# Kernel tuning notes

Hardware: AMD Instinct MI355X
Metric: run time of the kernel (lower is better)

The kernel has to match this reference:

```python
import jax, jax.numpy as jnp
import numpy as np

NUM_USERS, NUM_ITEMS, D = 100000, 200000, 128
B, LLEN, SLEN = 4096, 200, 50
NEG = -1e9


def setup_inputs() -> dict:
    key = jax.random.key(0)
    ks = jax.random.split(key, 10)
    w_range = float(np.sqrt(3.0 / D))
    return {
        "user_table": 0.01 * jax.random.normal(ks[0], (NUM_USERS, D), dtype=jnp.float32),
        "item_table": 0.01 * jax.random.normal(ks[1], (NUM_ITEMS, D), dtype=jnp.float32),
        "W1": jax.random.uniform(ks[2], (2 * D, 16), minval=-w_range, maxval=w_range, dtype=jnp.float32),
        "b1": jnp.zeros((16,), dtype=jnp.float32),
        "W2": jax.random.uniform(ks[3], (16, 1), minval=-w_range, maxval=w_range, dtype=jnp.float32),
        "b2": jnp.zeros((1,), dtype=jnp.float32),
        "user_inputs": jax.random.randint(ks[4], (B,), 0, NUM_USERS, dtype=jnp.int64) if jax.config.jax_enable_x64 else jax.random.randint(ks[4], (B,), 0, NUM_USERS, dtype=jnp.int32),
        "L_inputs": jax.random.randint(ks[5], (B, LLEN), 0, NUM_ITEMS, dtype=jnp.int32),
        "S_inputs": jax.random.randint(ks[6], (B, SLEN), 0, NUM_ITEMS, dtype=jnp.int32),
        "item_inputs": jax.random.randint(ks[7], (B,), 0, NUM_ITEMS, dtype=jnp.int32),
    }


def reference(user_table, item_table, W1, b1, W2, b2,
              user_inputs, L_inputs, S_inputs, item_inputs):
    def att_logits(x):  # x: [..., 2D] -> [...]
        h = jax.nn.relu(x @ W1 + b1)
        return (h @ W2 + b2)[..., 0]

    def masked_softmax(logits, mask):  # softmax over last axis restricted to mask
        logits = jnp.where(mask, logits, NEG)
        return jax.nn.softmax(logits, axis=-1)

    u_emb = user_table[user_inputs]                      # [B, D]

    # ---- long-term attention over L history ----
    L_mask = L_inputs >= 0                               # [B, L]
    L_idx = jnp.where(L_mask, L_inputs, 0)
    L_emb = item_table[L_idx]                            # [B, L, D]
    uL = jnp.concatenate([jnp.broadcast_to(u_emb[:, None, :], L_emb.shape), L_emb], axis=-1)  # [B, L, 2D]
    w1 = masked_softmax(att_logits(uL), L_mask)          # [B, L]
    u_long = jnp.einsum('bl,bld->bd', w1, L_emb)         # [B, D]

    # ---- short-term attention over [u_long] + S (L assumed nonempty) ----
    S_mask = S_inputs >= 0                               # [B, S]
    S_idx = jnp.where(S_mask, S_inputs, 0)
    S_emb = item_table[S_idx]                            # [B, S, D]
    seq = jnp.concatenate([u_long[:, None, :], S_emb], axis=1)   # [B, 1+S, D]
    seq_mask = jnp.concatenate([jnp.ones((seq.shape[0], 1), dtype=bool), S_mask], axis=1)
    uSeq = jnp.concatenate([jnp.broadcast_to(u_emb[:, None, :], seq.shape), seq], axis=-1)  # [B, 1+S, 2D]
    w2 = masked_softmax(att_logits(uSeq), seq_mask)      # [B, 1+S]
    user_hybrid = jnp.einsum('bs,bsd->bd', w2, seq)      # [B, D]

    # ---- score: bmm([B,1,D], [B,D,1]) -> [B,1,1] ----
    item_emb = item_table[item_inputs]                   # [B, D]
    score = jnp.sum(user_hybrid * item_emb, axis=-1)[:, None, None]
    return score
```

## Files before the change

### kernel.cpp

```cpp
#include <hip/hip_runtime.h>
#include <math.h>
#include <stdint.h>

#define D 128
#define LLEN 200
#define SLEN 50

typedef __attribute__((ext_vector_type(8))) short short8;
typedef __attribute__((ext_vector_type(4))) float f32x4;
typedef __attribute__((address_space(3))) unsigned int lds_uint;
typedef __attribute__((address_space(1))) unsigned int gbl_uint;

__device__ __forceinline__ unsigned short f2bf(float f) {
  unsigned int u = __float_as_uint(f);
  return (unsigned short)((u + 0x7FFFu + ((u >> 16) & 1u)) >> 16);
}

__device__ __forceinline__ float wave_red_sum(float v) {
#pragma unroll
  for (int m = 32; m >= 1; m >>= 1) v += __shfl_xor(v, m, 64);
  return v;
}
__device__ __forceinline__ float block_sum(float v, float* red) {
  v = wave_red_sum(v);
  if ((threadIdx.x & 63) == 0) red[threadIdx.x >> 6] = v;
  __syncthreads();
  v = red[0] + red[1] + red[2] + red[3];
  __syncthreads();
  return v;
}

#define STAGE(ROWARR, RBASE, IT, ROFF)                                        \
  do {                                                                        \
    const int s_ = tid + (IT) * 256;                                          \
    const int rr_ = (s_ >> 5) + (ROFF);                                       \
    int gid_ = ROWARR[(RBASE) + (s_ >> 5)];                                   \
    if (gid_ < 0) gid_ = 0;                                                   \
    const float4* src_ = &it4[(size_t)gid_ * 32 + ((s_ & 31) ^ (rr_ & 7))];   \
    __builtin_amdgcn_global_load_lds(                                         \
        (const gbl_uint*)(uintptr_t)src_,                                     \
        (lds_uint*)(uintptr_t)(&ebuf[((tid & 192) + (IT) * 256) * 4 +         \
                                     (ROFF) * 128]),                          \
        16, 0, 0);                                                            \
  } while (0)

#define FMA4(WL, P, ACC)                \
  do {                                  \
    ACC.x = fmaf((WL), P.x, ACC.x);     \
    ACC.y = fmaf((WL), P.y, ACC.y);     \
    ACC.z = fmaf((WL), P.z, ACC.z);     \
  } while (0);                          \
  ACC.w = fmaf((WL), P.w, ACC.w)

template <int MODE>
__device__ __forceinline__ void mfma_logits(
    const float* eb, const unsigned short* w1t,
    int w, int lane, float upart_j, float w2j, float b2v,
    const int* rowm, int nvalid, float* w_sh, float& pacc) {
  const int jj = lane & 15, ko = lane >> 4;
  const int x = lane & 7;
  const int q0 = (2 * ko) ^ x, q1 = q0 ^ 1;
  const int row = 16 * w + jj;
  const float4* rp = reinterpret_cast<const float4*>(&eb[row * 128]);
  const unsigned short* wp = &w1t[jj * 136 + 8 * ko];
  f32x4 acc = {0.f, 0.f, 0.f, 0.f};
#pragma unroll 1
  for (int s = 0; s < 4; ++s) {
    float4 fa = rp[q0 + 8 * s];
    float4 fb = rp[q1 + 8 * s];
    short8 bfrag = *reinterpret_cast<const short8*>(wp + 32 * s);
    short8 afrag;
    afrag[0] = (short)f2bf(fa.x); afrag[1] = (short)f2bf(fa.y);
    afrag[2] = (short)f2bf(fa.z); afrag[3] = (short)f2bf(fa.w);
    afrag[4] = (short)f2bf(fb.x); afrag[5] = (short)f2bf(fb.y);
    afrag[6] = (short)f2bf(fb.z); afrag[7] = (short)f2bf(fb.w);
    acc = __builtin_amdgcn_mfma_f32_16x16x32_bf16(afrag, bfrag, acc, 0, 0, 0);
  }
  float v0 = fmaxf(upart_j + acc[0], 0.f) * w2j;
  float v1 = fmaxf(upart_j + acc[1], 0.f) * w2j;
  float v2 = fmaxf(upart_j + acc[2], 0.f) * w2j;
  float v3 = fmaxf(upart_j + acc[3], 0.f) * w2j;
#pragma unroll
  for (int m = 1; m <= 8; m <<= 1) {
    v0 += __shfl_xor(v0, m, 64);
    v1 += __shfl_xor(v1, m, 64);
    v2 += __shfl_xor(v2, m, 64);
    v3 += __shfl_xor(v3, m, 64);
  }
  if ((lane & 15) == 0) {
    const int it0 = 16 * w + 4 * (lane >> 4);
    float p0, p1, p2, p3;
    if (MODE == 0) {
      p0 = (it0 + 0 < nvalid && rowm[it0 + 0] >= 0) ? expf(v0 + b2v) : 0.f;
      p1 = (it0 + 1 < nvalid && rowm[it0 + 1] >= 0) ? expf(v1 + b2v) : 0.f;
      p2 = (it0 + 2 < nvalid && rowm[it0 + 2] >= 0) ? expf(v2 + b2v) : 0.f;
      p3 = (it0 + 3 < nvalid && rowm[it0 + 3] >= 0) ? expf(v3 + b2v) : 0.f;
    } else {
      p0 = (it0 == 0) ? expf(v0 + b2v)
                      : ((it0 < nvalid && rowm[it0 - 1] >= 0) ? expf(v0 + b2v) : 0.f);
      p1 = (it0 + 1 < nvalid && rowm[it0 + 0] >= 0) ? expf(v1 + b2v) : 0.f;
      p2 = (it0 + 2 < nvalid && rowm[it0 + 1] >= 0) ? expf(v2 + b2v) : 0.f;
      p3 = (it0 + 3 < nvalid && rowm[it0 + 2] >= 0) ? expf(v3 + b2v) : 0.f;
    }
    float4 pv;
    pv.x = p0; pv.y = p1; pv.z = p2; pv.w = p3;
    reinterpret_cast<float4*>(w_sh)[it0 >> 2] = pv;
    pacc += p0 + p1 + p2 + p3;
  }
}

__global__ void __launch_bounds__(256, 4) din_kernel(
    const float* __restrict__ user_table, const float* __restrict__ item_table,
    const float* __restrict__ W1, const float* __restrict__ b1,
    const float* __restrict__ W2, const float* __restrict__ b2,
    const int* __restrict__ user_inputs, const int* __restrict__ L_inputs,
    const int* __restrict__ S_inputs, const int* __restrict__ item_inputs,
    float* __restrict__ out) {
  __shared__ __align__(16) float ebuf[64 * 128];
  __shared__ __align__(16) unsigned short w1t_sh[16 * 136];
  __shared__ __align__(16) float w_sh[64];
  __shared__ int rows1[LLEN];
  __shared__ int rowsS[SLEN];
  __shared__ float upart_sh[16];
  __shared__ float red_sh[4];

  const int b = blockIdx.x;
  const int tid = threadIdx.x;
  const int lane = tid & 63;
  const int w = __builtin_amdgcn_readfirstlane(tid >> 6);
  const int col4 = tid & 31;
  const int grp = tid >> 5;
  const float4* it4 = reinterpret_cast<const float4*>(item_table);

  const int urow = user_inputs[b];
  const float item_f =
      (tid < D) ? item_table[(size_t)item_inputs[b] * D + tid] : 0.f;
  if (tid < LLEN) rows1[tid] = L_inputs[(size_t)b * LLEN + tid];
  if (tid < SLEN) rowsS[tid] = S_inputs[(size_t)b * SLEN + tid];
  __syncthreads();

  STAGE(rows1, 0, 0, 0); STAGE(rows1, 0, 1, 0); STAGE(rows1, 0, 2, 0);
  STAGE(rows1, 0, 3, 0); STAGE(rows1, 0, 4, 0); STAGE(rows1, 0, 5, 0);
  STAGE(rows1, 0, 6, 0); STAGE(rows1, 0, 7, 0);

  {
    const int j = tid & 15, g = tid >> 4;
    const float* up = &user_table[(size_t)urow * D + 8 * g];
    const float* wp = &W1[(size_t)(8 * g) * 16 + j];
    float p = 0.f;
#pragma unroll
    for (int t = 0; t < 8; ++t) p = fmaf(up[t], wp[t * 16], p);
    p += __shfl_xor(p, 16, 64);
    p += __shfl_xor(p, 32, 64);
    if (lane < 16) w_sh[w * 16 + lane] = p;
  }
#pragma unroll
  for (int i = 0; i < 8; ++i) {
    int idx = tid + i * 256;
    int j = idx & 15, k = idx >> 4;
    w1t_sh[j * 136 + k] = f2bf(W1[(size_t)(128 + k) * 16 + j]);
  }
  __syncthreads();
  if (tid < 16)
    upart_sh[tid] = b1[tid] + w_sh[tid] + w_sh[16 + tid] + w_sh[32 + tid] +
                    w_sh[48 + tid];
  __syncthreads();

  const float b2v = b2[0];
  const float upart_j = upart_sh[lane & 15];
  const float w2j = W2[lane & 15];

  float pacc = 0.f;
  float4 uacc = make_float4(0.f, 0.f, 0.f, 0.f);

#pragma unroll 1
  for (int c = 0; c < 3; ++c) {
    mfma_logits<0>(ebuf, w1t_sh, w, lane, upart_j, w2j, b2v,
                   rows1 + c * 64, 64, w_sh, pacc);
    __syncthreads();
#pragma unroll
    for (int i = 0; i < 8; ++i) {
      int l = grp + 8 * i;
      float wl = w_sh[l];
      const float4 e = reinterpret_cast<const float4*>(&ebuf[l * 128])[col4 ^ grp];
      FMA4(wl, e, uacc);
    }
    __syncthreads();
    if (c < 2) {
      const int nb = c * 64 + 64;
      STAGE(rows1, nb, 0, 0); STAGE(rows1, nb, 1, 0); STAGE(rows1, nb, 2, 0);
      STAGE(rows1, nb, 3, 0); STAGE(rows1, nb, 4, 0); STAGE(rows1, nb, 5, 0);
      STAGE(rows1, nb, 6, 0); STAGE(rows1, nb, 7, 0);
    } else {
      STAGE(rows1, 192, 0, 0);
      STAGE(rowsS, 0, 1, 1); STAGE(rowsS, 0, 2, 1); STAGE(rowsS, 0, 3, 1);
      STAGE(rowsS, 0, 4, 1); STAGE(rowsS, 0, 5, 1);
      if (tid < 64) STAGE(rowsS, 0, 6, 1);
    }
    __syncthreads();
  }

  if (w == 0)
    mfma_logits<0>(ebuf, w1t_sh, w, lane, upart_j, w2j, b2v,
                   rows1 + 192, 8, w_sh, pacc);
  __syncthreads();
  {
    float wl = w_sh[grp];
    const float4 e = reinterpret_cast<const float4*>(&ebuf[grp * 128])[col4 ^ grp];
    FMA4(wl, e, uacc);
  }
  __syncthreads();
  STAGE(rowsS, 0, 0, 1);

  const float invS1 = 1.f / block_sum(pacc, red_sh);
  uacc.x += __shfl_xor(uacc.x, 32, 64);
  uacc.y += __shfl_xor(uacc.y, 32, 64);
  uacc.z += __shfl_xor(uacc.z, 32, 64);
  uacc.w += __shfl_xor(uacc.w, 32, 64);
  float* scr = &ebuf[52 * 128];
  if (lane < 32) reinterpret_cast<float4*>(scr)[(w << 5) + lane] = uacc;
  __syncthreads();
  if (tid < D) {
    float s = scr[tid] + scr[128 + tid] + scr[256 + tid] + scr[384 + tid];
    ebuf[tid] = s * invS1;
  }
  __syncthreads();

  float pacc2 = 0.f;
  mfma_logits<1>(ebuf, w1t_sh, w, lane, upart_j, w2j, b2v,
                 rowsS, 51, w_sh, pacc2);
  const float invS2 = 1.f / block_sum(pacc2, red_sh);

  float4 uacc2 = make_float4(0.f, 0.f, 0.f, 0.f);
#pragma unroll
  for (int i = 0; i < 6; ++i) {
    int l = grp + 8 * i;
    float wl = w_sh[l];
    const float4 e = reinterpret_cast<const float4*>(&ebuf[l * 128])[col4 ^ grp];
    FMA4(wl, e, uacc2);
  }
  if (grp < 3) {
    int l = 48 + grp;
    float wl = w_sh[l];
    const float4 e = reinterpret_cast<const float4*>(&ebuf[l * 128])[col4 ^ grp];
    FMA4(wl, e, uacc2);
  }

  uacc2.x += __shfl_xor(uacc2.x, 32, 64);
  uacc2.y += __shfl_xor(uacc2.y, 32, 64);
  uacc2.z += __shfl_xor(uacc2.z, 32, 64);
  uacc2.w += __shfl_xor(uacc2.w, 32, 64);
  if (lane < 32) reinterpret_cast<float4*>(scr)[(w << 5) + lane] = uacc2;
  __syncthreads();

  float sv = 0.f;
  if (tid < D) {
    float s = scr[tid] + scr[128 + tid] + scr[256 + tid] + scr[384 + tid];
    sv = s * invS2 * item_f;
  }
  float tot = block_sum(sv, red_sh);
  if (tid == 0) out[b] = tot;
}

extern "C" void kernel_launch(void* const* d_in, const int* in_sizes, int n_in,
                              void* d_out, int out_size, void* d_ws, size_t ws_size,
                              hipStream_t stream) {
  const float* user_table = (const float*)d_in[0];
  const float* item_table = (const float*)d_in[1];
  const float* W1 = (const float*)d_in[2];
  const float* b1 = (const float*)d_in[3];
  const float* W2 = (const float*)d_in[4];
  const float* b2 = (const float*)d_in[5];
  const int* user_inputs = (const int*)d_in[6];
  const int* L_inputs = (const int*)d_in[7];
  const int* S_inputs = (const int*)d_in[8];
  const int* item_inputs = (const int*)d_in[9];
  float* out = (float*)d_out;

  const int B = in_sizes[6];
  din_kernel<<<B, 256, 0, stream>>>(user_table, item_table, W1, b1, W2, b2,
                                    user_inputs, L_inputs, S_inputs, item_inputs,
                                    out);
}
```

Baseline: 254.9 us.

## Shrink LDS row buffer to 51 rows, process L history in four 50-row chunks

The shared embedding buffer shrinks from 64 to 51 rows, so the 200-long history is now staged and processed in four chunks of 50. This removes the separate 8-row tail pass, and the short-term S rows are staged only after the long-term pass finishes. The smaller LDS footprint plus launch bounds raised to 5 blocks per CU aim to increase occupancy and hide gather latency. In exchange the S-row gather no longer overlaps the last L chunk, some extra barriers are added, and the MFMA rows past 50 are clamped to redundant reads.

```diff
diff --git a/kernel.cpp b/kernel.cpp
--- a/kernel.cpp
+++ b/kernel.cpp
@@ -5,6 +5,8 @@
 #define D 128
 #define LLEN 200
 #define SLEN 50
+#define CH 50
+#define TROWS 51
 
 typedef __attribute__((ext_vector_type(8))) short short8;
 typedef __attribute__((ext_vector_type(4))) float f32x4;
@@ -44,6 +46,14 @@
         16, 0, 0);                                                            \
   } while (0)
 
+#define STAGE_CHUNK(RB)                                                \
+  do {                                                                 \
+    STAGE(rows1, RB, 0, 0); STAGE(rows1, RB, 1, 0);                    \
+    STAGE(rows1, RB, 2, 0); STAGE(rows1, RB, 3, 0);                    \
+    STAGE(rows1, RB, 4, 0); STAGE(rows1, RB, 5, 0);                    \
+    if (tid < 64) STAGE(rows1, RB, 6, 0);                              \
+  } while (0)
+
 #define FMA4(WL, P, ACC)                \
   do {                                  \
     ACC.x = fmaf((WL), P.x, ACC.x);     \
@@ -61,7 +71,8 @@
   const int x = lane & 7;
   const int q0 = (2 * ko) ^ x, q1 = q0 ^ 1;
   const int row = 16 * w + jj;
-  const float4* rp = reinterpret_cast<const float4*>(&eb[row * 128]);
+  const int rowc = (row <= 50) ? row : 50;
+  const float4* rp = reinterpret_cast<const float4*>(&eb[rowc * 128]);
   const unsigned short* wp = &w1t[jj * 136 + 8 * ko];
   f32x4 acc = {0.f, 0.f, 0.f, 0.f};
 #pragma unroll 1
@@ -109,14 +120,14 @@
   }
 }
 
-__global__ void __launch_bounds__(256, 4) din_kernel(
+__global__ void __launch_bounds__(256, 5) din_kernel(
     const float* __restrict__ user_table, const float* __restrict__ item_table,
     const float* __restrict__ W1, const float* __restrict__ b1,
     const float* __restrict__ W2, const float* __restrict__ b2,
     const int* __restrict__ user_inputs, const int* __restrict__ L_inputs,
     const int* __restrict__ S_inputs, const int* __restrict__ item_inputs,
     float* __restrict__ out) {
-  __shared__ __align__(16) float ebuf[64 * 128];
+  __shared__ __align__(16) float ebuf[TROWS * 128];
   __shared__ __align__(16) unsigned short w1t_sh[16 * 136];
   __shared__ __align__(16) float w_sh[64];
   __shared__ int rows1[LLEN];
@@ -131,6 +142,7 @@
   const int col4 = tid & 31;
   const int grp = tid >> 5;
   const float4* it4 = reinterpret_cast<const float4*>(item_table);
+  float* scr = &ebuf[0];
 
   const int urow = user_inputs[b];
   const float item_f =
@@ -139,9 +151,7 @@
   if (tid < SLEN) rowsS[tid] = S_inputs[(size_t)b * SLEN + tid];
   __syncthreads();
 
-  STAGE(rows1, 0, 0, 0); STAGE(rows1, 0, 1, 0); STAGE(rows1, 0, 2, 0);
-  STAGE(rows1, 0, 3, 0); STAGE(rows1, 0, 4, 0); STAGE(rows1, 0, 5, 0);
-  STAGE(rows1, 0, 6, 0); STAGE(rows1, 0, 7, 0);
+  STAGE_CHUNK(0);
 
   {
     const int j = tid & 15, g = tid >> 4;
@@ -174,56 +184,45 @@
   float4 uacc = make_float4(0.f, 0.f, 0.f, 0.f);
 
 #pragma unroll 1
-  for (int c = 0; c < 3; ++c) {
+  for (int c = 0; c < 4; ++c) {
     mfma_logits<0>(ebuf, w1t_sh, w, lane, upart_j, w2j, b2v,
-                   rows1 + c * 64, 64, w_sh, pacc);
+                   rows1 + c * CH, CH, w_sh, pacc);
     __syncthreads();
 #pragma unroll
-    for (int i = 0; i < 8; ++i) {
+    for (int i = 0; i < 6; ++i) {
       int l = grp + 8 * i;
       float wl = w_sh[l];
       const float4 e = reinterpret_cast<const float4*>(&ebuf[l * 128])[col4 ^ grp];
       FMA4(wl, e, uacc);
     }
-    __syncthreads();
-    if (c < 2) {
-      const int nb = c * 64 + 64;
-      STAGE(rows1, nb, 0, 0); STAGE(rows1, nb, 1, 0); STAGE(rows1, nb, 2, 0);
-      STAGE(rows1, nb, 3, 0); STAGE(rows1, nb, 4, 0); STAGE(rows1, nb, 5, 0);
-      STAGE(rows1, nb, 6, 0); STAGE(rows1, nb, 7, 0);
-    } else {
-      STAGE(rows1, 192, 0, 0);
-      STAGE(rowsS, 0, 1, 1); STAGE(rowsS, 0, 2, 1); STAGE(rowsS, 0, 3, 1);
-      STAGE(rowsS, 0, 4, 1); STAGE(rowsS, 0, 5, 1);
-      if (tid < 64) STAGE(rowsS, 0, 6, 1);
-    }
-    __syncthreads();
-  }
-
-  if (w == 0)
-    mfma_logits<0>(ebuf, w1t_sh, w, lane, upart_j, w2j, b2v,
-                   rows1 + 192, 8, w_sh, pacc);
-  __syncthreads();
-  {
-    float wl = w_sh[grp];
-    const float4 e = reinterpret_cast<const float4*>(&ebuf[grp * 128])[col4 ^ grp];
-    FMA4(wl, e, uacc);
-  }
-  __syncthreads();
-  STAGE(rowsS, 0, 0, 1);
+    if (grp < 2) {
+      int l = 48 + grp;
+      float wl = w_sh[l];
+      const float4 e = reinterpret_cast<const float4*>(&ebuf[l * 128])[col4 ^ grp];
+      FMA4(wl, e, uacc);
+    }
+    if (c < 3) {
+      __syncthreads();
+      STAGE_CHUNK((c + 1) * CH);
+      __syncthreads();
+    }
+  }
 
   const float invS1 = 1.f / block_sum(pacc, red_sh);
   uacc.x += __shfl_xor(uacc.x, 32, 64);
   uacc.y += __shfl_xor(uacc.y, 32, 64);
   uacc.z += __shfl_xor(uacc.z, 32, 64);
   uacc.w += __shfl_xor(uacc.w, 32, 64);
-  float* scr = &ebuf[52 * 128];
   if (lane < 32) reinterpret_cast<float4*>(scr)[(w << 5) + lane] = uacc;
   __syncthreads();
-  if (tid < D) {
-    float s = scr[tid] + scr[128 + tid] + scr[256 + tid] + scr[384 + tid];
-    ebuf[tid] = s * invS1;
-  }
+  float ulv = 0.f;
+  if (tid < D)
+    ulv = (scr[tid] + scr[128 + tid] + scr[256 + tid] + scr[384 + tid]) * invS1;
+  __syncthreads();
+  if (tid < D) ebuf[tid] = ulv;
+  STAGE(rowsS, 0, 0, 1); STAGE(rowsS, 0, 1, 1); STAGE(rowsS, 0, 2, 1);
+  STAGE(rowsS, 0, 3, 1); STAGE(rowsS, 0, 4, 1); STAGE(rowsS, 0, 5, 1);
+  if (tid < 64) STAGE(rowsS, 0, 6, 1);
   __syncthreads();
 
   float pacc2 = 0.f;
@@ -250,6 +249,7 @@
   uacc2.y += __shfl_xor(uacc2.y, 32, 64);
   uacc2.z += __shfl_xor(uacc2.z, 32, 64);
   uacc2.w += __shfl_xor(uacc2.w, 32, 64);
+  __syncthreads();
   if (lane < 32) reinterpret_cast<float4*>(scr)[(w << 5) + lane] = uacc2;
   __syncthreads();
 
```

Measured after the change: 248.5 us. 1.03x faster.
